# Performance work log

Hardware: AMD Instinct MI355X
Metric: run time of the kernel (lower is better)

Reference implementation:

```python
import jax, jax.numpy as jnp
import numpy as np

B, T, V, D, H, C = 64, 512, 50000, 128, 256, 50


def setup_inputs() -> dict:
    key = jax.random.key(0)
    ks = jax.random.split(key, 15)
    s = 0.05
    rn = lambda k, shape: jax.random.normal(k, shape, jnp.float32) * s
    words = jax.random.randint(ks[0], (B, T), 0, V)
    target = jax.random.randint(ks[1], (B, T), 0, C)
    seq_len = jax.random.randint(ks[2], (B,), T // 2, T + 1)
    seq_len = seq_len.at[0].set(T)  # ensure at least one full-length sequence
    return dict(
        words=words, target=target, seq_len=seq_len,
        emb=rn(ks[3], (V, D)),
        W_ih_f=rn(ks[4], (4 * H, D)), W_hh_f=rn(ks[5], (4 * H, H)), b_f=rn(ks[6], (4 * H,)),
        W_ih_b=rn(ks[7], (4 * H, D)), W_hh_b=rn(ks[8], (4 * H, H)), b_b=rn(ks[9], (4 * H,)),
        fc_W=rn(ks[10], (C, 2 * H)), fc_b=rn(ks[11], (C,)),
        trans=rn(ks[12], (C, C)), start_s=rn(ks[13], (C,)), end_s=rn(ks[14], (C,)),
    )


def _lstm(x, W_ih, W_hh, b):
    # unidirectional LSTM, PyTorch gate order (i, f, g, o). x: [B,T,D] -> h: [B,T,H]
    Hh = W_hh.shape[1]
    xg = jnp.einsum('btd,gd->btg', x, W_ih) + b  # [B,T,4H]

    def step(carry, xt):
        h, c = carry
        g = xt + h @ W_hh.T
        i, f, gg, o = jnp.split(g, 4, axis=-1)
        c = jax.nn.sigmoid(f) * c + jax.nn.sigmoid(i) * jnp.tanh(gg)
        h = jax.nn.sigmoid(o) * jnp.tanh(c)
        return (h, c), h

    h0 = jnp.zeros((x.shape[0], Hh), x.dtype)
    _, hs = jax.lax.scan(step, (h0, h0), jnp.swapaxes(xg, 0, 1))
    return jnp.swapaxes(hs, 0, 1)


def _rev_idx(seq_len, t_len):
    # per-sequence time-reversal indices (packed-sequence semantics for the backward LSTM)
    t = jnp.arange(t_len)[None, :]
    L = seq_len[:, None]
    return jnp.where(t < L, L - 1 - t, t)


def _bilstm_crf_loss(words, target, seq_len, emb, W_ih_f, W_hh_f, b_f,
                     W_ih_b, W_hh_b, b_b, fc_W, fc_b, trans, start_s, end_s):
    x = emb[words]  # [B,T,D]
    h_f = _lstm(x, W_ih_f, W_hh_f, b_f)
    idx = _rev_idx(seq_len, x.shape[1])
    x_rev = jnp.take_along_axis(x, idx[:, :, None], axis=1)
    h_b = jnp.take_along_axis(_lstm(x_rev, W_ih_b, W_hh_b, b_b), idx[:, :, None], axis=1)
    feats = jnp.concatenate([h_f, h_b], axis=-1) @ fc_W.T + fc_b  # [B,T,C]
    logits = jax.nn.log_softmax(feats, axis=-1)
    mask = jnp.arange(x.shape[1])[None, :] < seq_len[:, None]  # [B,T] bool

    # --- CRF normalizer (forward algorithm) ---
    alpha0 = logits[:, 0] + start_s  # [B,C]

    def step(alpha, inp):
        emit_t, m_t = inp  # [B,C], [B]
        tmp = alpha[:, :, None] + trans[None, :, :] + emit_t[:, None, :]
        new = jax.nn.logsumexp(tmp, axis=1)
        return jnp.where(m_t[:, None], new, alpha), None

    alpha, _ = jax.lax.scan(step, alpha0,
                            (jnp.swapaxes(logits, 0, 1)[1:], jnp.swapaxes(mask, 0, 1)[1:]))
    norm = jax.nn.logsumexp(alpha + end_s, axis=1)  # [B]

    # --- gold path score ---
    maskf = mask.astype(logits.dtype)
    emit = jnp.take_along_axis(logits, target[:, :, None], axis=2)[..., 0]  # [B,T]
    trans_sc = trans[target[:, :-1], target[:, 1:]]  # [B,T-1]
    last = target[jnp.arange(target.shape[0]), seq_len - 1]
    gold = (emit * maskf).sum(1) + (trans_sc * maskf[:, 1:]).sum(1) \
           + start_s[target[:, 0]] + end_s[last]

    return jnp.mean(norm - gold)


def reference(words, target, seq_len, emb, W_ih_f, W_hh_f, b_f,
              W_ih_b, W_hh_b, b_b, fc_W, fc_b, trans, start_s, end_s):
    return _bilstm_crf_loss(words, target, seq_len, emb, W_ih_f, W_hh_f, b_f,
                            W_ih_b, W_hh_b, b_b, fc_W, fc_b, trans, start_s, end_s)
```

## Files before the change

kernel.cpp:

```cpp
#include <hip/hip_runtime.h>
#include <hip/hip_bf16.h>

#define BB 64
#define TT 512
#define DD 128
#define HH 256
#define G4 1024
#define CC 50

typedef __bf16 bf16x8 __attribute__((ext_vector_type(8)));
typedef float  f32x4  __attribute__((ext_vector_type(4)));
typedef _Float16 h16x2 __attribute__((ext_vector_type(2)));

#if defined(__has_builtin)
#if __has_builtin(__builtin_amdgcn_fdot2)
#define HAS_FDOT2 1
#endif
#endif

__device__ __forceinline__ float bl16(unsigned u) { return __uint_as_float(u << 16); }
__device__ __forceinline__ float bh16(unsigned u) { return __uint_as_float(u & 0xffff0000u); }

__device__ __forceinline__ float sigf(float x) {
    return 1.f / (1.f + __expf(-x));
}
__device__ __forceinline__ float tanh_s(float x) {
    float ax = fabsf(x);
    float e = __expf(-2.f * ax);
    float r = (1.f - e) / (1.f + e);
    return copysignf(r, x);
}

__device__ __forceinline__ float dot8(float acc, uint4 w, uint4 h) {
#ifdef HAS_FDOT2
    acc = __builtin_amdgcn_fdot2(__builtin_bit_cast(h16x2, w.x),
                                 __builtin_bit_cast(h16x2, h.x), acc, false);
    acc = __builtin_amdgcn_fdot2(__builtin_bit_cast(h16x2, w.y),
                                 __builtin_bit_cast(h16x2, h.y), acc, false);
    acc = __builtin_amdgcn_fdot2(__builtin_bit_cast(h16x2, w.z),
                                 __builtin_bit_cast(h16x2, h.z), acc, false);
    acc = __builtin_amdgcn_fdot2(__builtin_bit_cast(h16x2, w.w),
                                 __builtin_bit_cast(h16x2, h.w), acc, false);
#else
    {
        h16x2 a = __builtin_bit_cast(h16x2, w.x), b = __builtin_bit_cast(h16x2, h.x);
        acc = fmaf((float)a.x, (float)b.x, acc); acc = fmaf((float)a.y, (float)b.y, acc);
        a = __builtin_bit_cast(h16x2, w.y); b = __builtin_bit_cast(h16x2, h.y);
        acc = fmaf((float)a.x, (float)b.x, acc); acc = fmaf((float)a.y, (float)b.y, acc);
        a = __builtin_bit_cast(h16x2, w.z); b = __builtin_bit_cast(h16x2, h.z);
        acc = fmaf((float)a.x, (float)b.x, acc); acc = fmaf((float)a.y, (float)b.y, acc);
        a = __builtin_bit_cast(h16x2, w.w); b = __builtin_bit_cast(h16x2, h.w);
        acc = fmaf((float)a.x, (float)b.x, acc); acc = fmaf((float)a.y, (float)b.y, acc);
    }
#endif
    return acc;
}

__global__ __launch_bounds__(256) void k_cvt(
    const float* __restrict__ src, __hip_bfloat16* __restrict__ dst, int n)
{
    int i = (blockIdx.x * 256 + threadIdx.x) * 8;
    if (i + 8 <= n) {
        float4 a = *(const float4*)(src + i);
        float4 b = *(const float4*)(src + i + 4);
        __hip_bfloat16 o[8];
        o[0] = __float2bfloat16(a.x); o[1] = __float2bfloat16(a.y);
        o[2] = __float2bfloat16(a.z); o[3] = __float2bfloat16(a.w);
        o[4] = __float2bfloat16(b.x); o[5] = __float2bfloat16(b.y);
        o[6] = __float2bfloat16(b.z); o[7] = __float2bfloat16(b.w);
        *(uint4*)(dst + i) = *(const uint4*)o;
    }
}

__global__ __launch_bounds__(512) void k_pack(
    const float* __restrict__ Wf, const float* __restrict__ Wb,
    uint4* __restrict__ Wp)
{
    int blk = blockIdx.x;
    int half = blk & 1;
    int kc = (blk >> 1) & 31;
    int dir = blk >> 6;
    int j = threadIdx.x;
    int row = half * 512 + j;
    const float* src = (dir ? Wb : Wf) + (size_t)row * 256 + kc * 8;
    float4 a = *(const float4*)src;
    float4 b = *(const float4*)(src + 4);
    _Float16 o[8];
    o[0] = (_Float16)a.x; o[1] = (_Float16)a.y;
    o[2] = (_Float16)a.z; o[3] = (_Float16)a.w;
    o[4] = (_Float16)b.x; o[5] = (_Float16)b.y;
    o[6] = (_Float16)b.z; o[7] = (_Float16)b.w;
    Wp[((size_t)dir * 64 + kc * 2 + half) * 512 + j] = *(const uint4*)o;
}

__global__ __launch_bounds__(256) void k_xg(
    const int* __restrict__ words,
    const __hip_bfloat16* __restrict__ emb,
    const __hip_bfloat16* __restrict__ Wf, const float* __restrict__ bfv,
    const __hip_bfloat16* __restrict__ Wb, const float* __restrict__ bbv,
    __hip_bfloat16* __restrict__ xg)
{
    int blk = blockIdx.x;
    int m_tile = blk >> 5;
    int n_group = blk & 31;
    int wave = threadIdx.x >> 6;
    int lane = threadIdx.x & 63;
    int n_tile = n_group * 4 + wave;
    int n = lane & 15;
    int quad = lane >> 4;

    int gate_g = n_tile * 16 + n;
    int dir = gate_g >> 10;
    int gate = gate_g & 1023;
    const __hip_bfloat16* W    = dir ? Wb : Wf;
    const float*          bias = dir ? bbv : bfv;

    int btrow_a = m_tile * 16 + n;
    int word = words[btrow_a];
    const __hip_bfloat16* arow = emb + (size_t)word * DD + quad * 8;
    const __hip_bfloat16* brow = W + (size_t)gate * DD + quad * 8;

    f32x4 acc = {0.f, 0.f, 0.f, 0.f};
#pragma unroll
    for (int kf = 0; kf < 4; ++kf) {
        bf16x8 a = *(const bf16x8*)(arow + kf * 32);
        bf16x8 b = *(const bf16x8*)(brow + kf * 32);
        acc = __builtin_amdgcn_mfma_f32_16x16x32_bf16(a, b, acc, 0, 0, 0);
    }
    float bv = bias[gate];
    size_t dbase = (size_t)dir * (size_t)(BB * TT * G4);
#pragma unroll
    for (int r = 0; r < 4; ++r) {
        int row = m_tile * 16 + quad * 4 + r;
        xg[dbase + (size_t)row * G4 + gate] = __float2bfloat16(acc[r] + bv);
    }
}

__global__ __launch_bounds__(512, 2) void k_lstm(
    const __hip_bfloat16* __restrict__ xg,
    const uint4* __restrict__ Wp,
    const int* __restrict__ seq_len,
    __hip_bfloat16* __restrict__ hcat)
{
    int b = blockIdx.x & 63;
    int dir = blockIdx.x >> 6;
    int j = threadIdx.x;

    __shared__ __align__(16) uint4 wB_lds[7 * 512];
    __shared__ float gbuf[2][512];
    __shared__ __align__(16) _Float16 hbf[2][HH];

    const uint4* Wd = Wp + (size_t)dir * 64 * 512;

    uint4 wA[32];
#pragma unroll
    for (int kc = 0; kc < 32; ++kc) wA[kc] = Wd[(kc * 2 + 0) * 512 + j];
    uint4 wB0[8];
#pragma unroll
    for (int kc = 0; kc < 8; ++kc) wB0[kc] = Wd[(kc * 2 + 1) * 512 + j];
#pragma unroll
    for (int kc = 8; kc < 15; ++kc) wB_lds[(kc - 8) * 512 + j] = Wd[(kc * 2 + 1) * 512 + j];

    if (j < HH) hbf[0][j] = (_Float16)0.f;
    float c = 0.f;
    int L = seq_len[b];
    const __hip_bfloat16* xgb = xg + (size_t)dir * (size_t)(BB * TT * G4)
                                   + (size_t)b * TT * G4;

    int tc = dir ? (L - 1) : 0;
    float xv0 = __bfloat162float(xgb[(size_t)tc * G4 + j]);
    float xv1 = __bfloat162float(xgb[(size_t)tc * G4 + 512 + j]);
    __syncthreads();

    for (int t = 0; t < TT; ++t) {
        int cur = t & 1, nxt = cur ^ 1;
        int tn = t + 1;
        int tcn = dir ? ((tn < L) ? (L - 1 - tn) : tn) : tn;
        bool pf = (tn < TT);
        __hip_bfloat16 p0, p1;
        if (pf) {
            p0 = xgb[(size_t)tcn * G4 + j];
            p1 = xgb[(size_t)tcn * G4 + 512 + j];
        }

        uint4 s1[9];
#pragma unroll
        for (int i = 0; i < 9; ++i) s1[i] = Wd[((15 + i) * 2 + 1) * 512 + j];

        const uint4* hv4 = (const uint4*)&hbf[cur][0];
        float a0 = 0.f, a1 = 0.f;
#pragma unroll
        for (int kc = 0; kc < 8; ++kc) {
            uint4 hv = hv4[kc];
            a0 = dot8(a0, wA[kc], hv);
            a1 = dot8(a1, wB0[kc], hv);
        }
#pragma unroll
        for (int kc = 8; kc < 15; ++kc) {
            uint4 hv = hv4[kc];
            a0 = dot8(a0, wA[kc], hv);
            a1 = dot8(a1, wB_lds[(kc - 8) * 512 + j], hv);
        }
        uint4 s2[8];
#pragma unroll
        for (int i = 0; i < 8; ++i) s2[i] = Wd[((24 + i) * 2 + 1) * 512 + j];
#pragma unroll
        for (int kc = 15; kc < 24; ++kc) {
            uint4 hv = hv4[kc];
            a0 = dot8(a0, wA[kc], hv);
            a1 = dot8(a1, s1[kc - 15], hv);
        }
#pragma unroll
        for (int kc = 24; kc < 32; ++kc) {
            uint4 hv = hv4[kc];
            a0 = dot8(a0, wA[kc], hv);
            a1 = dot8(a1, s2[kc - 24], hv);
        }
        gbuf[0][j] = a0 + xv0;
        gbuf[1][j] = a1 + xv1;
        __syncthreads();

        if (j < HH) {
            float gi = gbuf[0][j],      gg = gbuf[1][j];
            float gf = gbuf[0][HH + j], go = gbuf[1][HH + j];
            float i_ = sigf(gi), f_ = sigf(gf), G = tanh_s(gg), o_ = sigf(go);
            c = f_ * c + i_ * G;
            float h = o_ * tanh_s(c);
            hbf[nxt][j] = (_Float16)h;
            hcat[((size_t)(b * TT + tc)) * (2 * HH) + dir * HH + j] = __float2bfloat16(h);
        }
        if (pf) { xv0 = __bfloat162float(p0); xv1 = __bfloat162float(p1); }
        tc = tcn;
        __syncthreads();
    }
}

__global__ __launch_bounds__(64) void k_fc(
    const __hip_bfloat16* __restrict__ hcat,
    const __hip_bfloat16* __restrict__ fcW,
    const float* __restrict__ fcb,
    float* __restrict__ logits)
{
    int row = blockIdx.x;
    int tid = threadIdx.x;
    __shared__ __align__(16) float hrow[2 * HH];
    __shared__ float fbuf[CC + 2];

    {
        uint4 v = *(const uint4*)(hcat + (size_t)row * (2 * HH) + tid * 8);
        float* d = &hrow[tid * 8];
        d[0] = bl16(v.x); d[1] = bh16(v.x);
        d[2] = bl16(v.y); d[3] = bh16(v.y);
        d[4] = bl16(v.z); d[5] = bh16(v.z);
        d[6] = bl16(v.w); d[7] = bh16(v.w);
    }
    __syncthreads();

    if (tid < CC) {
        float acc = fcb[tid];
        const uint4* wr = (const uint4*)(fcW + (size_t)tid * (2 * HH));
#pragma unroll 8
        for (int kc = 0; kc < 64; ++kc) {
            uint4 wv = wr[kc];
            float4 h0 = *(const float4*)&hrow[kc * 8];
            float4 h1 = *(const float4*)&hrow[kc * 8 + 4];
            acc = fmaf(bl16(wv.x), h0.x, acc); acc = fmaf(bh16(wv.x), h0.y, acc);
            acc = fmaf(bl16(wv.y), h0.z, acc); acc = fmaf(bh16(wv.y), h0.w, acc);
            acc = fmaf(bl16(wv.z), h1.x, acc); acc = fmaf(bh16(wv.z), h1.y, acc);
            acc = fmaf(bl16(wv.w), h1.z, acc); acc = fmaf(bh16(wv.w), h1.w, acc);
        }
        fbuf[tid] = acc;
    }
    __syncthreads();

    float m = -1e30f;
    for (int i = 0; i < CC; ++i) m = fmaxf(m, fbuf[i]);
    float s = 0.f;
    for (int i = 0; i < CC; ++i) s += __expf(fbuf[i] - m);
    float lns = __logf(s);
    if (tid < CC) logits[(size_t)row * CC + tid] = fbuf[tid] - m - lns;
}

__global__ __launch_bounds__(256) void k_crf(
    const float* __restrict__ logits,
    const int* __restrict__ target,
    const int* __restrict__ seq_len,
    const float* __restrict__ trans,
    const float* __restrict__ start_s,
    const float* __restrict__ end_s,
    float* __restrict__ loss_b)
{
    const float L2E = 1.4426950408889634f;
    const float LN2 = 0.6931471805599453f;
    int b = blockIdx.x;
    int tid = threadIdx.x;
    int q = tid >> 6;
    int j = tid & 63;
    bool act = (j < CC);
    int L = seq_len[b];
    const float* lg = logits + (size_t)b * TT * CC;

    __shared__ float alpha2[64];
    __shared__ float mpart[4][64];
    __shared__ float spart[4][64];
    __shared__ float red[256];
    __shared__ float nbuf[CC + 2];

    int i0 = q * 13;
    int icnt = min(13, CC - i0);
    float treg[13];
    if (act) {
#pragma unroll
        for (int s = 0; s < 13; ++s)
            if (s < icnt) treg[s] = L2E * trans[(i0 + s) * CC + j];
    }
    if (q == 0 && act) alpha2[j] = L2E * (lg[j] + start_s[j]);
    __syncthreads();

    float v[13];
    for (int t = 1; t < L; ++t) {
        float mq = -1e30f;
        if (act) {
#pragma unroll
            for (int s = 0; s < 13; ++s)
                if (s < icnt) { v[s] = alpha2[i0 + s] + treg[s]; mq = fmaxf(mq, v[s]); }
        }
        mpart[q][j] = mq;
        __syncthreads();
        float M = fmaxf(fmaxf(mpart[0][j], mpart[1][j]), fmaxf(mpart[2][j], mpart[3][j]));
        float sq = 0.f;
        if (act) {
#pragma unroll
            for (int s = 0; s < 13; ++s)
                if (s < icnt) sq += exp2f(v[s] - M);
        }
        spart[q][j] = sq;
        __syncthreads();
        if (q == 0 && act) {
            float S = spart[0][j] + spart[1][j] + spart[2][j] + spart[3][j];
            alpha2[j] = M + log2f(S) + L2E * lg[(size_t)t * CC + j];
        }
        __syncthreads();
    }

    if (q == 0 && act) nbuf[j] = alpha2[j] + L2E * end_s[j];

    float gp = 0.f;
    const int* tg = target + b * TT;
    for (int t = tid; t < TT; t += 256) {
        if (t < L) {
            int c = tg[t];
            gp += lg[(size_t)t * CC + c];
            if (t >= 1) gp += trans[tg[t - 1] * CC + c];
        }
    }
    red[tid] = gp;
    __syncthreads();

    if (tid == 0) {
        float m2 = -1e30f;
        for (int i = 0; i < CC; ++i) m2 = fmaxf(m2, nbuf[i]);
        float s2 = 0.f;
        for (int i = 0; i < CC; ++i) s2 += exp2f(nbuf[i] - m2);
        float norm_nat = (m2 + log2f(s2)) * LN2;
        float g = 0.f;
        for (int i = 0; i < 256; ++i) g += red[i];
        g += start_s[tg[0]] + end_s[tg[L - 1]];
        loss_b[b] = norm_nat - g;
    }
}

__global__ void k_fin(const float* __restrict__ loss_b, float* __restrict__ out)
{
    int t = threadIdx.x;
    float v = loss_b[t];
#pragma unroll
    for (int o = 32; o > 0; o >>= 1) v += __shfl_down(v, o);
    if (t == 0) out[0] = v * (1.f / BB);
}

extern "C" void kernel_launch(void* const* d_in, const int* in_sizes, int n_in,
                              void* d_out, int out_size, void* d_ws, size_t ws_size,
                              hipStream_t stream)
{
    const int* words   = (const int*)d_in[0];
    const int* target  = (const int*)d_in[1];
    const int* seq_len = (const int*)d_in[2];
    const float* emb    = (const float*)d_in[3];
    const float* W_ih_f = (const float*)d_in[4];
    const float* W_hh_f = (const float*)d_in[5];
    const float* b_f    = (const float*)d_in[6];
    const float* W_ih_b = (const float*)d_in[7];
    const float* W_hh_b = (const float*)d_in[8];
    const float* b_b    = (const float*)d_in[9];
    const float* fc_W   = (const float*)d_in[10];
    const float* fc_b   = (const float*)d_in[11];
    const float* trans  = (const float*)d_in[12];
    const float* start_s= (const float*)d_in[13];
    const float* end_s  = (const float*)d_in[14];

    char* ws = (char*)d_ws;
    __hip_bfloat16* xg     = (__hip_bfloat16*)ws;
    __hip_bfloat16* hcat   = (__hip_bfloat16*)(ws + 134217728);
    float*          logits = (float*)(ws + 167772160);
    uint4*          Wp     = (uint4*)(ws + 167772160);
    float*          loss_b = (float*)(ws + 174325760);
    __hip_bfloat16* emb_bf = (__hip_bfloat16*)(ws + 174326016);
    __hip_bfloat16* wih_f  = (__hip_bfloat16*)(ws + 187126016);
    __hip_bfloat16* wih_b  = (__hip_bfloat16*)(ws + 187912448);
    __hip_bfloat16* fcw_bf = (__hip_bfloat16*)(ws + 188698880);

    k_cvt<<<3125, 256, 0, stream>>>(emb,    emb_bf, 6400000);
    k_cvt<<<64,   256, 0, stream>>>(W_ih_f, wih_f,  131072);
    k_cvt<<<64,   256, 0, stream>>>(W_ih_b, wih_b,  131072);
    k_cvt<<<13,   256, 0, stream>>>(fc_W,   fcw_bf, 25600);
    k_pack<<<128, 512, 0, stream>>>(W_hh_f, W_hh_b, Wp);

    k_xg  <<<65536, 256, 0, stream>>>(words, emb_bf, wih_f, b_f, wih_b, b_b, xg);
    k_lstm<<<128, 512, 0, stream>>>(xg, Wp, seq_len, hcat);
    k_fc  <<<32768, 64, 0, stream>>>(hcat, fcw_bf, fc_b, logits);
    k_crf <<<64, 256, 0, stream>>>(logits, target, seq_len, trans, start_s, end_s, loss_b);
    k_fin <<<1, 64, 0, stream>>>(loss_b, (float*)d_out);
}
```

Baseline: 2.072 ms.

## Retile input-gate GEMM with LDS-staged embeddings and drop full embedding conversion

Result: faster. 1.892 ms (-8.7%).

```diff
diff --git a/kernel.cpp b/kernel.cpp
--- a/kernel.cpp
+++ b/kernel.cpp
@@ -93,50 +93,73 @@
     Wp[((size_t)dir * 64 + kc * 2 + half) * 512 + j] = *(const uint4*)o;
 }
 
-__global__ __launch_bounds__(256) void k_xg(
+__global__ __launch_bounds__(256, 2) void k_xg(
     const int* __restrict__ words,
-    const __hip_bfloat16* __restrict__ emb,
-    const __hip_bfloat16* __restrict__ Wf, const float* __restrict__ bfv,
-    const __hip_bfloat16* __restrict__ Wb, const float* __restrict__ bbv,
+    const float* __restrict__ embf,
+    const __hip_bfloat16* __restrict__ Wih,
+    const float* __restrict__ bfv, const float* __restrict__ bbv,
     __hip_bfloat16* __restrict__ xg)
 {
-    int blk = blockIdx.x;
-    int m_tile = blk >> 5;
-    int n_group = blk & 31;
-    int wave = threadIdx.x >> 6;
-    int lane = threadIdx.x & 63;
-    int n_tile = n_group * 4 + wave;
-    int n = lane & 15;
-    int quad = lane >> 4;
-
-    int gate_g = n_tile * 16 + n;
-    int dir = gate_g >> 10;
-    int gate = gate_g & 1023;
-    const __hip_bfloat16* W    = dir ? Wb : Wf;
-    const float*          bias = dir ? bbv : bfv;
-
-    int btrow_a = m_tile * 16 + n;
-    int word = words[btrow_a];
-    const __hip_bfloat16* arow = emb + (size_t)word * DD + quad * 8;
-    const __hip_bfloat16* brow = W + (size_t)gate * DD + quad * 8;
-
-    f32x4 acc = {0.f, 0.f, 0.f, 0.f};
-#pragma unroll
-    for (int kf = 0; kf < 4; ++kf) {
-        bf16x8 a = *(const bf16x8*)(arow + kf * 32);
-        bf16x8 b = *(const bf16x8*)(brow + kf * 32);
-        acc = __builtin_amdgcn_mfma_f32_16x16x32_bf16(a, b, acc, 0, 0, 0);
-    }
-    float bv = bias[gate];
-    size_t dbase = (size_t)dir * (size_t)(BB * TT * G4);
-#pragma unroll
-    for (int r = 0; r < 4; ++r) {
-        int row = m_tile * 16 + quad * 4 + r;
-        xg[dbase + (size_t)row * G4 + gate] = __float2bfloat16(acc[r] + bv);
-    }
-}
-
-__global__ __launch_bounds__(512, 2) void k_lstm(
+    __shared__ __align__(16) __hip_bfloat16 A[64][136];
+    int tid = threadIdx.x;
+    int bt0 = blockIdx.x * 64;
+
+    {
+        int r = tid >> 2;
+        int c0 = (tid & 3) * 32;
+        int word = words[bt0 + r];
+        const float* src = embf + (size_t)word * DD + c0;
+#pragma unroll
+        for (int i = 0; i < 8; ++i) {
+            float4 v = *(const float4*)(src + i * 4);
+            __hip_bfloat16 o[4] = {__float2bfloat16(v.x), __float2bfloat16(v.y),
+                                   __float2bfloat16(v.z), __float2bfloat16(v.w)};
+            *(uint2*)&A[r][c0 + i * 4] = *(const uint2*)o;
+        }
+    }
+    __syncthreads();
+
+    int wave = tid >> 6, lane = tid & 63;
+    int m = lane & 15, quad = lane >> 4;
+
+    bf16x8 afr[4][4];
+#pragma unroll
+    for (int ms = 0; ms < 4; ++ms)
+#pragma unroll
+        for (int kf = 0; kf < 4; ++kf)
+            afr[ms][kf] = *(const bf16x8*)&A[ms * 16 + m][quad * 8 + kf * 32];
+
+#pragma unroll 1
+    for (int i = 0; i < 32; ++i) {
+        int nt = wave * 32 + i;
+        int gate_g = nt * 16 + m;
+        int dir = gate_g >> 10;
+        int gate = gate_g & 1023;
+        const __hip_bfloat16* brow = Wih + (size_t)gate_g * DD + quad * 8;
+        bf16x8 bfr[4];
+#pragma unroll
+        for (int kf = 0; kf < 4; ++kf) bfr[kf] = *(const bf16x8*)(brow + kf * 32);
+        float bv = dir ? bbv[gate] : bfv[gate];
+        size_t dbase = (size_t)dir * (size_t)(BB * TT * G4);
+
+#pragma unroll
+        for (int ms = 0; ms < 4; ++ms) {
+            f32x4 acc = {0.f, 0.f, 0.f, 0.f};
+#pragma unroll
+            for (int kf = 0; kf < 4; ++kf)
+                acc = __builtin_amdgcn_mfma_f32_16x16x32_bf16(afr[ms][kf], bfr[kf], acc, 0, 0, 0);
+#pragma unroll
+            for (int r = 0; r < 4; ++r) {
+                int btrow = bt0 + ms * 16 + quad * 4 + r;
+                xg[dbase + (size_t)btrow * G4 + gate] = __float2bfloat16(acc[r] + bv);
+            }
+        }
+    }
+}
+
+__global__ __launch_bounds__(512)
+__attribute__((amdgpu_waves_per_eu(2, 2)))
+void k_lstm(
     const __hip_bfloat16* __restrict__ xg,
     const uint4* __restrict__ Wp,
     const int* __restrict__ seq_len,
@@ -405,18 +428,15 @@
     float*          logits = (float*)(ws + 167772160);
     uint4*          Wp     = (uint4*)(ws + 167772160);
     float*          loss_b = (float*)(ws + 174325760);
-    __hip_bfloat16* emb_bf = (__hip_bfloat16*)(ws + 174326016);
-    __hip_bfloat16* wih_f  = (__hip_bfloat16*)(ws + 187126016);
-    __hip_bfloat16* wih_b  = (__hip_bfloat16*)(ws + 187912448);
-    __hip_bfloat16* fcw_bf = (__hip_bfloat16*)(ws + 188698880);
-
-    k_cvt<<<3125, 256, 0, stream>>>(emb,    emb_bf, 6400000);
-    k_cvt<<<64,   256, 0, stream>>>(W_ih_f, wih_f,  131072);
-    k_cvt<<<64,   256, 0, stream>>>(W_ih_b, wih_b,  131072);
-    k_cvt<<<13,   256, 0, stream>>>(fc_W,   fcw_bf, 25600);
+    __hip_bfloat16* wihall = (__hip_bfloat16*)(ws + 174326016);
+    __hip_bfloat16* fcw_bf = (__hip_bfloat16*)(ws + 174850304);
+
+    k_cvt<<<64,  256, 0, stream>>>(W_ih_f, wihall,          131072);
+    k_cvt<<<64,  256, 0, stream>>>(W_ih_b, wihall + 131072, 131072);
+    k_cvt<<<13,  256, 0, stream>>>(fc_W,   fcw_bf,          25600);
     k_pack<<<128, 512, 0, stream>>>(W_hh_f, W_hh_b, Wp);
 
-    k_xg  <<<65536, 256, 0, stream>>>(words, emb_bf, wih_f, b_f, wih_b, b_b, xg);
+    k_xg  <<<512, 256, 0, stream>>>(words, emb, wihall, b_f, b_b, xg);
     k_lstm<<<128, 512, 0, stream>>>(xg, Wp, seq_len, hcat);
     k_fc  <<<32768, 64, 0, stream>>>(hcat, fcw_bf, fc_b, logits);
     k_crf <<<64, 256, 0, stream>>>(logits, target, seq_len, trans, start_s, end_s, loss_b);
```
